# Kernel tuning notes

Measured on AMD Instinct MI355X. Metric: run time of the kernel, lower is better.

Reference implementation:

```python
import jax, jax.numpy as jnp
import numpy as np

MARGIN = 0.09
SCALE_POS = 2.0
SCALE_NEG = 40.0
EPS = 1e-05
THRESH1 = 0.501
THRESH2 = 0.531


def setup_inputs() -> dict:
    key = jax.random.key(0)
    k1, k2 = jax.random.split(key)
    B, D, N_CLASSES = 4096, 1024, 64
    feats = jax.random.normal(k1, (B, D), dtype=jnp.float32)
    # thresholds in the loss assume cosine-scale similarities -> L2 normalize
    feats = feats / jnp.linalg.norm(feats, axis=1, keepdims=True)
    labels = jax.random.randint(k2, (B,), 0, N_CLASSES, dtype=jnp.int64)
    return {"feats": feats, "labels": labels}


def reference(feats, labels):
    B = feats.shape[0]
    sim = jnp.matmul(feats, feats.T)  # [B, B]
    eq = labels[:, None] == labels[None, :]
    neg_mask = ~eq
    pos_mask = eq & (sim < 1.0 - EPS)  # drops self-similarity (~1)
    # per-row max over negatives; rows with no negatives -> -inf -> no pos survive
    max_neg = jnp.max(jnp.where(neg_mask, sim, -jnp.inf), axis=1)  # [B]
    pos_mask = pos_mask & ((sim - MARGIN) < max_neg[:, None])
    n_pos = jnp.sum(pos_mask, axis=1)
    n_neg = jnp.sum(neg_mask, axis=1)
    pos_sum = jnp.sum(jnp.where(pos_mask, jnp.exp(-SCALE_POS * sim), 0.0), axis=1)
    neg_sum = jnp.sum(jnp.where(neg_mask, jnp.exp(SCALE_NEG * sim), 0.0), axis=1)
    pos_loss = (1.0 / SCALE_POS) * jnp.log(
        (pos_sum + np.exp(-SCALE_POS * THRESH1)) / (n_pos + 1.0))
    neg_loss = (1.0 / SCALE_NEG) * jnp.log(
        (neg_sum + np.exp(SCALE_NEG * THRESH2)) / (n_neg + 1.0))
    per_row = jnp.log(5.33 + jnp.exp(pos_loss + neg_loss))  # [B]
    valid = (n_neg >= 1) & (n_pos >= 1)
    return jnp.sum(jnp.where(valid, per_row, 0.0)) / B
```

## Files before the change

kernel.cpp:

```cpp
#include <hip/hip_runtime.h>
#include <hip/hip_bf16.h>
#include <math.h>

typedef __attribute__((ext_vector_type(4))) float floatx4;

#define MARGIN_C    0.09f
#define ONE_M_EPS   0.99999f
#define NCLS        64
#define MEMSTRIDE   256

__device__ __forceinline__ unsigned short f2bf(float f) {
    unsigned u = __float_as_uint(f);
    u += 0x7fffu + ((u >> 16) & 1u);
    return (unsigned short)(u >> 16);
}
__device__ __forceinline__ float bf2f(unsigned short v) {
    return __uint_as_float(((unsigned)v) << 16);
}
__device__ __forceinline__ unsigned fkey(float f) {
    unsigned u = __float_as_uint(f);
    return (u >> 31) ? ~u : (u | 0x80000000u);
}
__device__ __forceinline__ float fdec(unsigned k) {
    return __uint_as_float((k >> 31) ? (k & 0x7fffffffu) : ~k);
}
__device__ __forceinline__ void gld16(const void* g, void* l) {
    __builtin_amdgcn_global_load_lds(
        (const __attribute__((address_space(1))) void*)g,
        (__attribute__((address_space(3))) void*)l, 16, 0, 0);
}

__global__ __launch_bounds__(256) void cvt_build(const float* __restrict__ in,
                                                 unsigned* __restrict__ out8,
                                                 float* __restrict__ statz,
                                                 const int* __restrict__ labels,
                                                 int* __restrict__ members,
                                                 int* __restrict__ classCount,
                                                 float* __restrict__ loss_out,
                                                 int n4, int nz4, int ncvt, int Bn) {
    __shared__ int cnt;
    const int bid = blockIdx.x;
    const int t = threadIdx.x;
    if (bid < ncvt) {
        int i = bid * 256 + t;
        if (bid == 0 && t == 0) loss_out[0] = 0.0f;
        if (i < nz4) ((float4*)statz)[i] = make_float4(0.f, 0.f, 0.f, 0.f);
        if (i >= n4) return;
        float4 v = ((const float4*)in)[i];
        int w = __builtin_amdgcn_cvt_pk_fp8_f32(v.x, v.y, 0, false);
        w = __builtin_amdgcn_cvt_pk_fp8_f32(v.z, v.w, w, true);
        out8[i] = (unsigned)w;
    } else {
        const int c = bid - ncvt;
        if (t == 0) cnt = 0;
        __syncthreads();
        for (int j = t; j < Bn; j += 256) {
            if (labels[j] == c) {
                int p = atomicAdd(&cnt, 1);
                if (p < MEMSTRIDE) members[c * MEMSTRIDE + p] = j;
            }
        }
        __syncthreads();
        if (t == 0) classCount[c] = (cnt < MEMSTRIDE) ? cnt : MEMSTRIDE;
    }
}

__global__ __launch_bounds__(256, 4) void gemm_fused(const unsigned char* __restrict__ fb8,
                                                     const int* __restrict__ labels,
                                                     float* __restrict__ negsum,
                                                     unsigned* __restrict__ negmax,
                                                     unsigned short* __restrict__ pairsim,
                                                     int Bn, int Dn) {
    __shared__ __align__(16) unsigned char As[2][8192];
    __shared__ __align__(16) unsigned char Bs[2][4096];
    __shared__ int Lrow[128], Lcol[64];

    const int bid = blockIdx.x;
    int by = (int)(sqrtf((float)bid + 0.25f) - 0.5f);
    while ((by + 1) * (by + 2) <= bid) by++;
    while (by * (by + 1) > bid) by--;
    const int c64 = bid - by * (by + 1);
    const int gcb = c64 * 64;
    const bool mirror = (gcb < by * 128);

    const int t = threadIdx.x;
    const int wave = t >> 6, lane = t & 63;
    const int quad = lane >> 4, m16 = lane & 15;

    if (t < 128) Lrow[t] = labels[by * 128 + t];
    else if (t < 192) Lcol[t - 128] = labels[gcb + (t - 128)];

    const int r = t >> 2, a = t & 3;
    const int gofs = ((2 * a) ^ (r & 6)) * 8;
    const unsigned char* gA0 = fb8 + (size_t)(by * 128 + r) * Dn + gofs;
    const unsigned char* gA1 = gA0 + (size_t)64 * Dn;
    const unsigned char* gB0 = fb8 + (size_t)(gcb + r) * Dn + gofs;
    const int lb = t * 16;

    floatx4 acc[2][4];
#pragma unroll
    for (int i = 0; i < 2; i++)
#pragma unroll
        for (int j = 0; j < 4; j++) acc[i][j] = (floatx4){0.f, 0.f, 0.f, 0.f};

    const int fragA = (wave * 32 + m16) * 64;
    const int fragB = m16 * 64;
    const int sw = m16 & 6;
    const int sK0 = (quad ^ sw) * 8;
    const int sK1 = ((quad + 4) ^ sw) * 8;

    const int NS = Dn / 64;

    gld16(gA0, &As[0][lb]);
    gld16(gA1, &As[0][4096 + lb]);
    gld16(gB0, &Bs[0][lb]);
    __syncthreads();

    for (int s = 0; s < NS; s++) {
        if (s + 1 < NS) {
            const int ko = (s + 1) * 64;
            const int nb = (s + 1) & 1;
            gld16(gA0 + ko, &As[nb][lb]);
            gld16(gA1 + ko, &As[nb][4096 + lb]);
            gld16(gB0 + ko, &Bs[nb][lb]);
        }
        __builtin_amdgcn_sched_barrier(0);

        const unsigned char* as_ = &As[s & 1][0];
        const unsigned char* bs_ = &Bs[s & 1][0];
        long af[2], bfr[4];
#pragma unroll
        for (int i = 0; i < 2; i++) af[i]  = *(const long*)(as_ + fragA + i * 1024 + sK0);
#pragma unroll
        for (int j = 0; j < 4; j++) bfr[j] = *(const long*)(bs_ + fragB + j * 1024 + sK0);
#pragma unroll
        for (int i = 0; i < 2; i++)
#pragma unroll
            for (int j = 0; j < 4; j++)
                acc[i][j] = __builtin_amdgcn_mfma_f32_16x16x32_fp8_fp8(af[i], bfr[j], acc[i][j], 0, 0, 0);
#pragma unroll
        for (int i = 0; i < 2; i++) af[i]  = *(const long*)(as_ + fragA + i * 1024 + sK1);
#pragma unroll
        for (int j = 0; j < 4; j++) bfr[j] = *(const long*)(bs_ + fragB + j * 1024 + sK1);
#pragma unroll
        for (int i = 0; i < 2; i++)
#pragma unroll
            for (int j = 0; j < 4; j++)
                acc[i][j] = __builtin_amdgcn_mfma_f32_16x16x32_fp8_fp8(af[i], bfr[j], acc[i][j], 0, 0, 0);

        __syncthreads();
    }

    int cl[4], gc[4];
#pragma unroll
    for (int j = 0; j < 4; j++) {
        cl[j] = Lcol[j * 16 + m16];
        gc[j] = gcb + j * 16 + m16;
    }

    float nsm[4] = {0.f, 0.f, 0.f, 0.f};
    float nmm[4] = {-INFINITY, -INFINITY, -INFINITY, -INFINITY};

#pragma unroll
    for (int i = 0; i < 2; i++) {
#pragma unroll
        for (int rr = 0; rr < 4; rr++) {
            const int rowl = wave * 32 + i * 16 + quad * 4 + rr;
            const int rl = Lrow[rowl];
            const int gr = by * 128 + rowl;
            float ns = 0.f, nm = -INFINITY;
#pragma unroll
            for (int j = 0; j < 4; j++) {
                const float s = acc[i][j][rr];
                if (cl[j] != rl) {
                    const float e = __expf(40.f * s);
                    ns += e;
                    nm = fmaxf(nm, s);
                    nsm[j] += e;
                    nmm[j] = fmaxf(nmm[j], s);
                } else if ((gr != gc[j]) & (s < ONE_M_EPS)) {
                    const unsigned short v = f2bf(s);
                    pairsim[(size_t)gr * Bn + gc[j]] = v;
                    if (mirror) pairsim[(size_t)gc[j] * Bn + gr] = v;
                }
            }
#pragma unroll
            for (int o = 8; o; o >>= 1) {
                ns += __shfl_down(ns, o, 64);
                nm = fmaxf(nm, __shfl_down(nm, o, 64));
            }
            if (m16 == 0) {
                atomicAdd(negsum + gr, ns);
                atomicMax(negmax + gr, fkey(nm));
            }
        }
    }
    if (mirror) {
#pragma unroll
        for (int j = 0; j < 4; j++) {
            float v = nsm[j], m = nmm[j];
            v += __shfl_down(v, 16, 64);
            m = fmaxf(m, __shfl_down(m, 16, 64));
            v += __shfl_down(v, 32, 64);
            m = fmaxf(m, __shfl_down(m, 32, 64));
            if (quad == 0) {
                atomicAdd(negsum + gc[j], v);
                atomicMax(negmax + gc[j], fkey(m));
            }
        }
    }
}

__global__ __launch_bounds__(256) void pos_final(const unsigned short* __restrict__ pairsim,
                                                 const int* __restrict__ labels,
                                                 const int* __restrict__ members,
                                                 const int* __restrict__ classCount,
                                                 const unsigned* __restrict__ negmax,
                                                 const float* __restrict__ negsum,
                                                 float* __restrict__ out, int Bn) {
    __shared__ float part[4];
    const int t = threadIdx.x;
    const int wave = t >> 6, lane = t & 63;
    float wacc = 0.f;
#pragma unroll
    for (int rr = 0; rr < 4; rr++) {
        const int r = blockIdx.x * 16 + wave * 4 + rr;
        if (r >= Bn) break;
        const int lab = labels[r];
        const int n = classCount[lab];
        const int base = lab * MEMSTRIDE;
        const float mx = fdec(negmax[r]);
        const unsigned short* prow = pairsim + (size_t)r * Bn;

        float ps = 0.f, pc = 0.f;
        for (int j = lane; j < n; j += 64) {
            const int m = members[base + j];
            if (m != r) {
                const float s = bf2f(prow[m]);
                if ((s - MARGIN_C) < mx) {
                    ps += __expf(-2.f * s);
                    pc += 1.f;
                }
            }
        }
#pragma unroll
        for (int o = 32; o; o >>= 1) {
            ps += __shfl_down(ps, o, 64);
            pc += __shfl_down(pc, o, 64);
        }
        if (lane == 0) {
            const int nneg = Bn - n;
            if (nneg >= 1 && pc >= 0.5f) {
                float pl = 0.5f * logf((ps + expf(-2.f * 0.501f)) / (pc + 1.f));
                float nl = (1.f / 40.f) * logf((negsum[r] + expf(40.f * 0.531f)) / ((float)nneg + 1.f));
                wacc += logf(5.33f + expf(pl + nl));
            }
        }
    }
    if (lane == 0) part[wave] = wacc;
    __syncthreads();
    if (t == 0) {
        atomicAdd(out, (part[0] + part[1] + part[2] + part[3]) / (float)Bn);
    }
}

extern "C" void kernel_launch(void* const* d_in, const int* in_sizes, int n_in,
                              void* d_out, int out_size, void* d_ws, size_t ws_size,
                              hipStream_t stream) {
    const float* feats = (const float*)d_in[0];
    const int* labels  = (const int*)d_in[1];
    float* out = (float*)d_out;

    const int Bn = in_sizes[1];
    const int Dn = in_sizes[0] / Bn;

    unsigned char* fb8 = (unsigned char*)d_ws;
    float* stats    = (float*)(fb8 + (size_t)Bn * Dn);
    float* negsum   = stats;
    unsigned* negmax = (unsigned*)(stats + Bn);
    int* classCount = (int*)(stats + 2 * Bn);
    int* members    = classCount + NCLS;
    unsigned short* pairsim = (unsigned short*)(members + NCLS * MEMSTRIDE);

    const int n4   = (Bn * Dn) / 4;
    const int nz4  = (2 * Bn) / 4;
    const int ncvt = (n4 + 255) / 256;
    cvt_build<<<ncvt + NCLS, 256, 0, stream>>>(feats, (unsigned*)fb8, stats, labels,
                                               members, classCount, out,
                                               n4, nz4, ncvt, Bn);

    const int nt = Bn / 128;
    const int ngrid = nt * (nt + 1);
    gemm_fused<<<ngrid, 256, 0, stream>>>(fb8, labels, negsum, negmax, pairsim, Bn, Dn);

    pos_final<<<(Bn + 15) / 16, 256, 0, stream>>>(pairsim, labels, members, classCount,
                                                  negmax, negsum, out, Bn);
}
```

Baseline: 108.6 us.

## Store positive-pair similarities in compact per-row class-position buffer

Instead of scattering positive-pair similarities into a sparse B×B bf16 matrix, each sample gets its index within its class, and positive similarities are written to a dense [B, MEMSTRIDE] buffer. The final kernel reads contiguous rows without the members indirection, and now uses one wave per row. This replaces scattered strided writes and gathered reads across a large matrix with compact accesses. It adds a picls array and extra shared loads in the GEMM epilogue, and the pos_final grid assumes B is divisible by 4.

```diff
diff --git a/kernel.cpp b/kernel.cpp
--- a/kernel.cpp
+++ b/kernel.cpp
@@ -36,6 +36,7 @@
                                                  const int* __restrict__ labels,
                                                  int* __restrict__ members,
                                                  int* __restrict__ classCount,
+                                                 int* __restrict__ picls,
                                                  float* __restrict__ loss_out,
                                                  int n4, int nz4, int ncvt, int Bn) {
     __shared__ int cnt;
@@ -58,6 +59,7 @@
             if (labels[j] == c) {
                 int p = atomicAdd(&cnt, 1);
                 if (p < MEMSTRIDE) members[c * MEMSTRIDE + p] = j;
+                picls[j] = p;
             }
         }
         __syncthreads();
@@ -67,13 +69,15 @@
 
 __global__ __launch_bounds__(256, 4) void gemm_fused(const unsigned char* __restrict__ fb8,
                                                      const int* __restrict__ labels,
+                                                     const int* __restrict__ picls,
                                                      float* __restrict__ negsum,
                                                      unsigned* __restrict__ negmax,
-                                                     unsigned short* __restrict__ pairsim,
+                                                     unsigned short* __restrict__ posc,
                                                      int Bn, int Dn) {
     __shared__ __align__(16) unsigned char As[2][8192];
     __shared__ __align__(16) unsigned char Bs[2][4096];
     __shared__ int Lrow[128], Lcol[64];
+    __shared__ int Prow[128], Pcol[64];
 
     const int bid = blockIdx.x;
     int by = (int)(sqrtf((float)bid + 0.25f) - 0.5f);
@@ -87,8 +91,13 @@
     const int wave = t >> 6, lane = t & 63;
     const int quad = lane >> 4, m16 = lane & 15;
 
-    if (t < 128) Lrow[t] = labels[by * 128 + t];
-    else if (t < 192) Lcol[t - 128] = labels[gcb + (t - 128)];
+    if (t < 128) {
+        Lrow[t] = labels[by * 128 + t];
+        Prow[t] = picls[by * 128 + t];
+    } else if (t < 192) {
+        Lcol[t - 128] = labels[gcb + (t - 128)];
+        Pcol[t - 128] = picls[gcb + (t - 128)];
+    }
 
     const int r = t >> 2, a = t & 3;
     const int gofs = ((2 * a) ^ (r & 6)) * 8;
@@ -151,11 +160,12 @@
         __syncthreads();
     }
 
-    int cl[4], gc[4];
+    int cl[4], gc[4], pc_[4];
 #pragma unroll
     for (int j = 0; j < 4; j++) {
         cl[j] = Lcol[j * 16 + m16];
         gc[j] = gcb + j * 16 + m16;
+        pc_[j] = Pcol[j * 16 + m16];
     }
 
     float nsm[4] = {0.f, 0.f, 0.f, 0.f};
@@ -180,8 +190,13 @@
                     nmm[j] = fmaxf(nmm[j], s);
                 } else if ((gr != gc[j]) & (s < ONE_M_EPS)) {
                     const unsigned short v = f2bf(s);
-                    pairsim[(size_t)gr * Bn + gc[j]] = v;
-                    if (mirror) pairsim[(size_t)gc[j] * Bn + gr] = v;
+                    if (pc_[j] < MEMSTRIDE)
+                        posc[(size_t)gr * MEMSTRIDE + pc_[j]] = v;
+                    if (mirror) {
+                        const int pr_ = Prow[rowl];
+                        if (pr_ < MEMSTRIDE)
+                            posc[(size_t)gc[j] * MEMSTRIDE + pr_] = v;
+                    }
                 }
             }
 #pragma unroll
@@ -211,53 +226,50 @@
     }
 }
 
-__global__ __launch_bounds__(256) void pos_final(const unsigned short* __restrict__ pairsim,
+__global__ __launch_bounds__(256) void pos_final(const unsigned short* __restrict__ posc,
                                                  const int* __restrict__ labels,
-                                                 const int* __restrict__ members,
                                                  const int* __restrict__ classCount,
+                                                 const int* __restrict__ picls,
                                                  const unsigned* __restrict__ negmax,
                                                  const float* __restrict__ negsum,
                                                  float* __restrict__ out, int Bn) {
     __shared__ float part[4];
     const int t = threadIdx.x;
     const int wave = t >> 6, lane = t & 63;
+    const int r = blockIdx.x * 4 + wave;
+
+    const int lab = labels[r];
+    const int selfp = picls[r];
+    const float mx = fdec(negmax[r]);
+    const float nsum = negsum[r];
+    const int n = classCount[lab];
+    const unsigned short* prow = posc + (size_t)r * MEMSTRIDE;
+
+    float ps = 0.f, pc = 0.f;
+    for (int j = lane; j < n; j += 64) {
+        if (j != selfp) {
+            const float s = bf2f(prow[j]);
+            if ((s - MARGIN_C) < mx) {
+                ps += __expf(-2.f * s);
+                pc += 1.f;
+            }
+        }
+    }
+#pragma unroll
+    for (int o = 32; o; o >>= 1) {
+        ps += __shfl_down(ps, o, 64);
+        pc += __shfl_down(pc, o, 64);
+    }
     float wacc = 0.f;
-#pragma unroll
-    for (int rr = 0; rr < 4; rr++) {
-        const int r = blockIdx.x * 16 + wave * 4 + rr;
-        if (r >= Bn) break;
-        const int lab = labels[r];
-        const int n = classCount[lab];
-        const int base = lab * MEMSTRIDE;
-        const float mx = fdec(negmax[r]);
-        const unsigned short* prow = pairsim + (size_t)r * Bn;
-
-        float ps = 0.f, pc = 0.f;
-        for (int j = lane; j < n; j += 64) {
-            const int m = members[base + j];
-            if (m != r) {
-                const float s = bf2f(prow[m]);
-                if ((s - MARGIN_C) < mx) {
-                    ps += __expf(-2.f * s);
-                    pc += 1.f;
-                }
-            }
-        }
-#pragma unroll
-        for (int o = 32; o; o >>= 1) {
-            ps += __shfl_down(ps, o, 64);
-            pc += __shfl_down(pc, o, 64);
-        }
-        if (lane == 0) {
-            const int nneg = Bn - n;
-            if (nneg >= 1 && pc >= 0.5f) {
-                float pl = 0.5f * logf((ps + expf(-2.f * 0.501f)) / (pc + 1.f));
-                float nl = (1.f / 40.f) * logf((negsum[r] + expf(40.f * 0.531f)) / ((float)nneg + 1.f));
-                wacc += logf(5.33f + expf(pl + nl));
-            }
-        }
-    }
-    if (lane == 0) part[wave] = wacc;
+    if (lane == 0) {
+        const int nneg = Bn - n;
+        if (nneg >= 1 && pc >= 0.5f) {
+            float pl = 0.5f * logf((ps + expf(-2.f * 0.501f)) / (pc + 1.f));
+            float nl = (1.f / 40.f) * logf((nsum + expf(40.f * 0.531f)) / ((float)nneg + 1.f));
+            wacc = logf(5.33f + expf(pl + nl));
+        }
+        part[wave] = wacc;
+    }
     __syncthreads();
     if (t == 0) {
         atomicAdd(out, (part[0] + part[1] + part[2] + part[3]) / (float)Bn);
@@ -280,19 +292,20 @@
     unsigned* negmax = (unsigned*)(stats + Bn);
     int* classCount = (int*)(stats + 2 * Bn);
     int* members    = classCount + NCLS;
-    unsigned short* pairsim = (unsigned short*)(members + NCLS * MEMSTRIDE);
+    int* picls      = members + NCLS * MEMSTRIDE;
+    unsigned short* posc = (unsigned short*)(picls + Bn);
 
     const int n4   = (Bn * Dn) / 4;
     const int nz4  = (2 * Bn) / 4;
     const int ncvt = (n4 + 255) / 256;
     cvt_build<<<ncvt + NCLS, 256, 0, stream>>>(feats, (unsigned*)fb8, stats, labels,
-                                               members, classCount, out,
+                                               members, classCount, picls, out,
                                                n4, nz4, ncvt, Bn);
 
     const int nt = Bn / 128;
     const int ngrid = nt * (nt + 1);
-    gemm_fused<<<ngrid, 256, 0, stream>>>(fb8, labels, negsum, negmax, pairsim, Bn, Dn);
-
-    pos_final<<<(Bn + 15) / 16, 256, 0, stream>>>(pairsim, labels, members, classCount,
-                                                  negmax, negsum, out, Bn);
-}
+    gemm_fused<<<ngrid, 256, 0, stream>>>(fb8, labels, picls, negsum, negmax, posc, Bn, Dn);
+
+    pos_final<<<Bn / 4, 256, 0, stream>>>(posc, labels, classCount, picls,
+                                          negmax, negsum, out, Bn);
+}
```

Result: slower. 114.5 us (+5.4%).
